# Kernel optimization log

Hardware: AMD Instinct MI355X
Metric: run time of the kernel (lower is better)

The kernel has to match this reference:

```python
import jax, jax.numpy as jnp
import numpy as np


def setup_inputs() -> dict:
    key = jax.random.key(0)
    ks = jax.random.split(key, 6)
    B, S, H, HD = 2, 2048, 2048, 128
    scale = 0.02
    return {
        "hidden_state": jax.random.normal(ks[0], (B, S, H), jnp.float32),
        "attention_mask": jnp.ones((B, 1, 1, S), jnp.int32),
        "Wq": jax.random.normal(ks[1], (H, H), jnp.float32) * scale,
        "bq": jnp.zeros((H,), jnp.float32),
        "Wk": jax.random.normal(ks[2], (HD, H), jnp.float32) * scale,
        "bk": jnp.zeros((HD,), jnp.float32),
        "Wv": jax.random.normal(ks[3], (HD, H), jnp.float32) * scale,
        "bv": jnp.zeros((HD,), jnp.float32),
        "Wo": jax.random.normal(ks[4], (H, H), jnp.float32) * scale,
        "bo": jnp.zeros((H,), jnp.float32),
    }


def reference(hidden_state, attention_mask, Wq, bq, Wk, bk, Wv, bv, Wo, bo):
    B, S, H = hidden_state.shape
    hd = Wk.shape[0]          # head_dim (single shared KV head)
    nh = H // hd              # num query heads
    # projections (torch Linear: x @ W.T + b)
    q = (hidden_state @ Wq.T + bq).reshape(B, S, nh, hd).transpose(0, 2, 1, 3)  # (B,nh,S,hd)
    k = hidden_state @ Wk.T + bk   # (B,S,hd) shared head
    v = hidden_state @ Wv.T + bv   # (B,S,hd)
    scores = jnp.einsum('bhqd,bkd->bhqk', q, k) / jnp.sqrt(jnp.float32(hd))
    scores = jnp.where(attention_mask == 0, -jnp.inf, scores)
    probs = jax.nn.softmax(scores, axis=-1)
    # dropout p=0.0 -> identity (inference)
    out = jnp.einsum('bhqk,bkd->bhqd', probs, v)           # (B,nh,S,hd)
    out = out.transpose(0, 2, 1, 3).reshape(B, S, H)
    return out @ Wo.T + bo
```

## Files before the change

kernel.cpp:

```cpp
#include <hip/hip_runtime.h>

typedef unsigned short u16;
typedef unsigned int u32;
typedef __attribute__((ext_vector_type(8))) short bf16x8;
typedef __attribute__((ext_vector_type(4))) float f32x4;
typedef __attribute__((ext_vector_type(16))) float f32x16;

#define QSC 0.12751798f

__device__ __forceinline__ u16 f2bf(float f) {
  union { float f; unsigned u; } a; a.f = f;
  unsigned r = a.u + 0x7fffu + ((a.u >> 16) & 1u);
  return (u16)(r >> 16);
}

__device__ __forceinline__ void gload16(const void* g, void* l) {
  __builtin_amdgcn_global_load_lds(
      (const __attribute__((address_space(1))) unsigned int*)g,
      (__attribute__((address_space(3))) unsigned int*)l, 16, 0, 0);
}

__global__ __launch_bounds__(256) void cvt_all_k(
    const float* __restrict__ h, const float* __restrict__ wq,
    const float* __restrict__ wk, const float* __restrict__ wv,
    const float* __restrict__ wo, u16* __restrict__ hid,
    u16* __restrict__ wqkv, u16* __restrict__ wob) {
  int i = blockIdx.x * 256 + threadIdx.x;
  if (i >= 4325376) return;
  const float4* s;
  ushort4* d;
  if (i < 2097152) {
    s = (const float4*)h + i;              d = (ushort4*)hid + i;
  } else if (i < 3145728) {
    s = (const float4*)wq + (i - 2097152); d = (ushort4*)wqkv + (i - 2097152);
  } else if (i < 3211264) {
    s = (const float4*)wk + (i - 3145728);
    d = (ushort4*)(wqkv + 4194304) + (i - 3145728);
  } else if (i < 3276800) {
    s = (const float4*)wv + (i - 3211264);
    d = (ushort4*)(wqkv + 4456448) + (i - 3211264);
  } else {
    s = (const float4*)wo + (i - 3276800); d = (ushort4*)wob + (i - 3276800);
  }
  float4 v = *s;
  ushort4 o;
  o.x = f2bf(v.x); o.y = f2bf(v.y); o.z = f2bf(v.z); o.w = f2bf(v.w);
  *d = o;
}

template <int MODE>
__global__ __launch_bounds__(256) void gemm_bt_k(
    const u16* __restrict__ A, const u16* __restrict__ Bm,
    const float* __restrict__ bias0, const float* __restrict__ bias1,
    const float* __restrict__ bias2,
    float* __restrict__ outF, u16* __restrict__ outQ,
    u16* __restrict__ outK, u16* __restrict__ outVt,
    int M, int N, int K) {
  __shared__ u16 As[128 * 32];
  __shared__ u16 Bs[128 * 32];
  const int t = threadIdx.x;
  const int lane = t & 63, wid = t >> 6;
  const int m0 = blockIdx.y * 128, n0 = blockIdx.x * 128;
  const int wr = (wid >> 1) * 64, wc = (wid & 1) * 64;
  const int col = lane & 15, grp = lane >> 4;

  const int srow = t >> 2;
  const int sp = t & 3;
  const int sslot = (sp ^ ((srow >> 1) & 3)) * 8;
  const u16* aS0 = A + (size_t)(m0 + srow) * K + sslot;
  const u16* aS1 = A + (size_t)(m0 + srow + 64) * K + sslot;
  const u16* bS0 = Bm + (size_t)(n0 + srow) * K + sslot;
  const u16* bS1 = Bm + (size_t)(n0 + srow + 64) * K + sslot;
  u16* aD0 = As + t * 8; u16* aD1 = As + (256 + t) * 8;
  u16* bD0 = Bs + t * 8; u16* bD1 = Bs + (256 + t) * 8;

  f32x4 acc[4][4] = {};
  const int nk = K >> 5;
  for (int kt = 0; kt < nk; ++kt) {
    __syncthreads();
    const int ko = kt * 32;
    gload16(aS0 + ko, aD0);
    gload16(aS1 + ko, aD1);
    gload16(bS0 + ko, bD0);
    gload16(bS1 + ko, bD1);
    __syncthreads();
    bf16x8 af[4], bfr[4];
#pragma unroll
    for (int f = 0; f < 4; ++f) {
      int ra = wr + f * 16 + col;
      af[f] = *(const bf16x8*)(const void*)((const char*)As + ra * 64 +
                                            ((grp ^ ((ra >> 1) & 3)) << 4));
      int rb = wc + f * 16 + col;
      bfr[f] = *(const bf16x8*)(const void*)((const char*)Bs + rb * 64 +
                                             ((grp ^ ((rb >> 1) & 3)) << 4));
    }
    __builtin_amdgcn_s_setprio(1);
#pragma unroll
    for (int i = 0; i < 4; ++i)
#pragma unroll
      for (int j = 0; j < 4; ++j)
        acc[i][j] = __builtin_amdgcn_mfma_f32_16x16x32_bf16(af[i], bfr[j],
                                                            acc[i][j], 0, 0, 0);
    __builtin_amdgcn_s_setprio(0);
  }

#pragma unroll
  for (int i = 0; i < 4; ++i) {
    const int gmb = m0 + wr + i * 16 + grp * 4;
#pragma unroll
    for (int j = 0; j < 4; ++j) {
      const int gn = n0 + wc + j * 16 + col;
      float bv;
      if (MODE == 1) bv = bias0[gn];
      else bv = (gn < 2048) ? bias0[gn]
                            : (gn < 2176 ? bias1[gn - 2048] : bias2[gn - 2176]);
#pragma unroll
      for (int r = 0; r < 4; ++r) {
        const int gm = gmb + r;
        float val = acc[i][j][r] + bv;
        if (MODE == 1) {
          outF[(size_t)gm * N + gn] = val;
        } else {
          if (gn < 2048) {
            outQ[(size_t)gm * 2048 + gn] = f2bf(val * QSC);
          } else if (gn < 2176) {
            outK[(size_t)gm * 128 + (gn - 2048)] = f2bf(val);
          } else {
            const int b = gm >> 11, s = gm & 2047, d = gn - 2176;
            outVt[((size_t)(b * 128 + d) << 11) + s] = f2bf(val);
          }
        }
      }
    }
  }
}

__global__ __launch_bounds__(256, 2) void attn_k(const u16* __restrict__ Q,
                                                 const u16* __restrict__ Kb,
                                                 const u16* __restrict__ Vt,
                                                 u16* __restrict__ O) {
  __shared__ u16 Ks[2][64 * 128];
  __shared__ u16 Vs[2][128 * 64];
  const int t = threadIdx.x, lane = t & 63, w = t >> 6;
  const int qt = blockIdx.x & 15;
  const int h = (blockIdx.x >> 4) & 15;
  const int b = blockIdx.x >> 8;
  const int l31 = lane & 31, hi = lane >> 5;
  const int swl = l31 & 7;
  const int q0w = qt * 128 + w * 32;

  bf16x8 qf[8];
  {
    const u16* qp = Q + (size_t)(b * 2048 + q0w + l31) * 2048 + h * 128 + hi * 8;
#pragma unroll
    for (int kc = 0; kc < 8; ++kc) qf[kc] = *(const bf16x8*)(qp + kc * 16);
  }

  const int krow = t >> 4, kslot = t & 15;
  const int sig = (krow & 3) | ((krow & 4) << 1) | ((krow & 8) >> 1);
  const int vrow = t >> 3, vslot = t & 7;
  const u16* ksrc0 =
      Kb + (size_t)(b * 2048 + sig) * 128 + ((kslot ^ (krow & 7)) * 8);
  const u16* vsrc0 =
      Vt + (size_t)(b * 128 + vrow) * 2048 + ((vslot ^ (vrow & 7)) * 8);
  const int ldst = t * 8;

  auto STAGE_K = [&](int ktn, int nb) {
#pragma unroll
    for (int i = 0; i < 4; ++i)
      gload16(ksrc0 + i * 2048 + ktn * 8192, &Ks[nb][i * 2048 + ldst]);
  };
  auto STAGE_V = [&](int ktn, int nb) {
#pragma unroll
    for (int i = 0; i < 4; ++i)
      gload16(vsrc0 + (size_t)i * 65536 + ktn * 64, &Vs[nb][i * 2048 + ldst]);
  };

  STAGE_K(0, 0);
  STAGE_V(0, 0);
  STAGE_K(1, 1);
  __syncthreads();

  f32x16 st0 = {}, st1 = {};
#pragma unroll
  for (int kc = 0; kc < 8; ++kc) {
    const int sw = ((kc * 2 + hi) ^ swl) << 4;
    bf16x8 k0 = *(const bf16x8*)(const void*)((const char*)Ks[0] + l31 * 256 + sw);
    bf16x8 k1 = *(const bf16x8*)(const void*)((const char*)Ks[0] + (32 + l31) * 256 + sw);
    st0 = __builtin_amdgcn_mfma_f32_32x32x16_bf16(k0, qf[kc], st0, 0, 0, 0);
    st1 = __builtin_amdgcn_mfma_f32_32x32x16_bf16(k1, qf[kc], st1, 0, 0, 0);
  }
  STAGE_V(1, 1);
  __syncthreads();

  f32x16 of[4] = {};
  float mrun = -3e38f, lsum = 0.f;
  u32 pk[4][4];

  for (int tt = 0; tt < 31; ++tt) {
    if (tt < 30) STAGE_K(tt + 2, tt & 1);

    const char* kbase = (const char*)Ks[(tt + 1) & 1];
    const char* vbase = (const char*)Vs[tt & 1];
    f32x16 n0 = {}, n1 = {};
#pragma unroll
    for (int kc = 0; kc < 8; ++kc) {
      const int sw = ((kc * 2 + hi) ^ swl) << 4;
      bf16x8 k0 = *(const bf16x8*)(const void*)(kbase + l31 * 256 + sw);
      bf16x8 k1 = *(const bf16x8*)(const void*)(kbase + (32 + l31) * 256 + sw);
      n0 = __builtin_amdgcn_mfma_f32_32x32x16_bf16(k0, qf[kc], n0, 0, 0, 0);
      n1 = __builtin_amdgcn_mfma_f32_32x32x16_bf16(k1, qf[kc], n1, 0, 0, 0);
    }

    float m8[8];
#pragma unroll
    for (int i = 0; i < 8; ++i)
      m8[i] = fmaxf(fmaxf(st0[i], st0[i + 8]), fmaxf(st1[i], st1[i + 8]));
#pragma unroll
    for (int i = 0; i < 4; ++i) m8[i] = fmaxf(m8[i], m8[i + 4]);
    float mx = fmaxf(fmaxf(m8[0], m8[1]), fmaxf(m8[2], m8[3]));
    mx = fmaxf(mx, __shfl_xor(mx, 32));
    if (__any(mx > mrun + 8.f)) {
      float mnew = fmaxf(mrun, mx);
      float al = __builtin_amdgcn_exp2f(mrun - mnew);
      mrun = mnew;
      lsum *= al;
#pragma unroll
      for (int rr = 0; rr < 16; ++rr) {
        const int rho = (rr & 3) + 8 * (rr >> 2) + 4 * hi;
        float av = __shfl(al, (lane & 32) | rho);
#pragma unroll
        for (int dt = 0; dt < 4; ++dt) of[dt][rr] *= av;
      }
    }
    {
      float ps0 = 0.f, ps1 = 0.f;
#pragma unroll
      for (int a = 0; a < 8; ++a) {
        float e0 = __builtin_amdgcn_exp2f(st0[2 * a] - mrun);
        float e1 = __builtin_amdgcn_exp2f(st0[2 * a + 1] - mrun);
        float e2 = __builtin_amdgcn_exp2f(st1[2 * a] - mrun);
        float e3 = __builtin_amdgcn_exp2f(st1[2 * a + 1] - mrun);
        ps0 += (e0 + e1);
        ps1 += (e2 + e3);
        asm("v_cvt_pk_bf16_f32 %0, %1, %2" : "=v"(pk[a >> 2][a & 3]) : "v"(e0), "v"(e1));
        asm("v_cvt_pk_bf16_f32 %0, %1, %2" : "=v"(pk[2 + (a >> 2)][a & 3]) : "v"(e2), "v"(e3));
      }
      lsum += ps0 + ps1;
    }

    __builtin_amdgcn_s_setprio(1);
#pragma unroll
    for (int kvc = 0; kvc < 4; ++kvc) {
      union { u32 u[4]; bf16x8 v; } pu;
#pragma unroll
      for (int ww = 0; ww < 4; ++ww) pu.u[ww] = pk[kvc][ww];
      const int swv = ((kvc * 2 + hi) ^ swl) << 4;
#pragma unroll
      for (int dt = 0; dt < 4; ++dt) {
        bf16x8 vb = *(const bf16x8*)(const void*)(vbase + (dt * 32 + l31) * 128 + swv);
        of[dt] = __builtin_amdgcn_mfma_f32_32x32x16_bf16(pu.v, vb, of[dt], 0, 0, 0);
      }
    }
    __builtin_amdgcn_s_setprio(0);

    __syncthreads();
    if (tt < 30) STAGE_V(tt + 2, tt & 1);
    st0 = n0;
    st1 = n1;
  }

  {
    float m8[8];
#pragma unroll
    for (int i = 0; i < 8; ++i)
      m8[i] = fmaxf(fmaxf(st0[i], st0[i + 8]), fmaxf(st1[i], st1[i + 8]));
#pragma unroll
    for (int i = 0; i < 4; ++i) m8[i] = fmaxf(m8[i], m8[i + 4]);
    float mx = fmaxf(fmaxf(m8[0], m8[1]), fmaxf(m8[2], m8[3]));
    mx = fmaxf(mx, __shfl_xor(mx, 32));
    if (__any(mx > mrun + 8.f)) {
      float mnew = fmaxf(mrun, mx);
      float al = __builtin_amdgcn_exp2f(mrun - mnew);
      mrun = mnew;
      lsum *= al;
#pragma unroll
      for (int rr = 0; rr < 16; ++rr) {
        const int rho = (rr & 3) + 8 * (rr >> 2) + 4 * hi;
        float av = __shfl(al, (lane & 32) | rho);
#pragma unroll
        for (int dt = 0; dt < 4; ++dt) of[dt][rr] *= av;
      }
    }
    float ps = 0.f;
#pragma unroll
    for (int a = 0; a < 8; ++a) {
      float e0 = __builtin_amdgcn_exp2f(st0[2 * a] - mrun);
      float e1 = __builtin_amdgcn_exp2f(st0[2 * a + 1] - mrun);
      float e2 = __builtin_amdgcn_exp2f(st1[2 * a] - mrun);
      float e3 = __builtin_amdgcn_exp2f(st1[2 * a + 1] - mrun);
      ps += (e0 + e1) + (e2 + e3);
      asm("v_cvt_pk_bf16_f32 %0, %1, %2" : "=v"(pk[a >> 2][a & 3]) : "v"(e0), "v"(e1));
      asm("v_cvt_pk_bf16_f32 %0, %1, %2" : "=v"(pk[2 + (a >> 2)][a & 3]) : "v"(e2), "v"(e3));
    }
    lsum += ps;
    const char* vbase = (const char*)Vs[1];
    __builtin_amdgcn_s_setprio(1);
#pragma unroll
    for (int kvc = 0; kvc < 4; ++kvc) {
      union { u32 u[4]; bf16x8 v; } pu;
#pragma unroll
      for (int ww = 0; ww < 4; ++ww) pu.u[ww] = pk[kvc][ww];
      const int swv = ((kvc * 2 + hi) ^ swl) << 4;
#pragma unroll
      for (int dt = 0; dt < 4; ++dt) {
        bf16x8 vb = *(const bf16x8*)(const void*)(vbase + (dt * 32 + l31) * 128 + swv);
        of[dt] = __builtin_amdgcn_mfma_f32_32x32x16_bf16(pu.v, vb, of[dt], 0, 0, 0);
      }
    }
    __builtin_amdgcn_s_setprio(0);
  }

  float lt = lsum + __shfl_xor(lsum, 32);
  float inv = 1.0f / lt;
#pragma unroll
  for (int rr = 0; rr < 16; ++rr) {
    const int rho = (rr & 3) + 8 * (rr >> 2) + 4 * hi;
    float iv = __shfl(inv, (lane & 32) | rho);
    u16* orow = O + (size_t)(b * 2048 + q0w + rho) * 2048 + h * 128 + l31;
#pragma unroll
    for (int dt = 0; dt < 4; ++dt) orow[dt * 32] = f2bf(of[dt][rr] * iv);
  }
}

extern "C" void kernel_launch(void* const* d_in, const int* in_sizes, int n_in,
                              void* d_out, int out_size, void* d_ws,
                              size_t ws_size, hipStream_t stream) {
  const float* hidden = (const float*)d_in[0];
  const float* Wq = (const float*)d_in[2];
  const float* bq = (const float*)d_in[3];
  const float* Wk = (const float*)d_in[4];
  const float* bk = (const float*)d_in[5];
  const float* Wv = (const float*)d_in[6];
  const float* bv = (const float*)d_in[7];
  const float* Wo = (const float*)d_in[8];
  const float* bo = (const float*)d_in[9];
  float* out = (float*)d_out;

  char* ws = (char*)d_ws;
  u16* hid  = (u16*)(ws);
  u16* wqkv = (u16*)(ws + 16777216);
  u16* wo   = (u16*)(ws + 26214400);
  u16* q    = (u16*)(ws + 34603008);
  u16* kb   = (u16*)(ws + 51380224);
  u16* vt   = (u16*)(ws + 52428800);
  u16* attn = (u16*)(ws + 53477376);

  cvt_all_k<<<16896, 256, 0, stream>>>(hidden, Wq, Wk, Wv, Wo, hid, wqkv, wo);

  gemm_bt_k<0><<<dim3(18, 32), 256, 0, stream>>>(
      hid, wqkv, bq, bk, bv, nullptr, q, kb, vt, 4096, 2304, 2048);

  attn_k<<<512, 256, 0, stream>>>(q, kb, vt, attn);

  gemm_bt_k<1><<<dim3(16, 32), 256, 0, stream>>>(
      attn, wo, bo, nullptr, nullptr, out, nullptr, nullptr, nullptr,
      4096, 2048, 2048);
}
```

Before: 210.4 us.

## Load K tiles directly from global into registers instead of LDS staging

K tiles are no longer staged through shared memory. Each lane reads its K fragments straight from global memory into registers, prefetching the next tile right after the QK MFMAs. The software-pipelined QK-ahead structure and the peeled final iteration are removed, so each iteration now computes its own scores. This frees half the LDS and cuts LDS traffic, but it adds register pressure (16 extra bf16x8 fragments) and exposes global-load latency, which may now stall the next iteration's MFMAs.

After: 271.0 us. 1.29x slower.

```diff
diff --git a/kernel.cpp b/kernel.cpp
--- a/kernel.cpp
+++ b/kernel.cpp
@@ -139,7 +139,6 @@
                                                  const u16* __restrict__ Kb,
                                                  const u16* __restrict__ Vt,
                                                  u16* __restrict__ O) {
-  __shared__ u16 Ks[2][64 * 128];
   __shared__ u16 Vs[2][128 * 64];
   const int t = threadIdx.x, lane = t & 63, w = t >> 6;
   const int qt = blockIdx.x & 15;
@@ -156,40 +155,27 @@
     for (int kc = 0; kc < 8; ++kc) qf[kc] = *(const bf16x8*)(qp + kc * 16);
   }
 
-  const int krow = t >> 4, kslot = t & 15;
-  const int sig = (krow & 3) | ((krow & 4) << 1) | ((krow & 8) >> 1);
+  const int sigl = (l31 & 19) | ((l31 & 4) << 1) | ((l31 & 8) >> 1);
+  const u16* kp0 = Kb + (size_t)(b * 2048 + sigl) * 128 + hi * 8;
+  const u16* kp1 = kp0 + 32 * 128;
+
   const int vrow = t >> 3, vslot = t & 7;
-  const u16* ksrc0 =
-      Kb + (size_t)(b * 2048 + sig) * 128 + ((kslot ^ (krow & 7)) * 8);
   const u16* vsrc0 =
       Vt + (size_t)(b * 128 + vrow) * 2048 + ((vslot ^ (vrow & 7)) * 8);
   const int ldst = t * 8;
-
-  auto STAGE_K = [&](int ktn, int nb) {
-#pragma unroll
-    for (int i = 0; i < 4; ++i)
-      gload16(ksrc0 + i * 2048 + ktn * 8192, &Ks[nb][i * 2048 + ldst]);
-  };
   auto STAGE_V = [&](int ktn, int nb) {
 #pragma unroll
     for (int i = 0; i < 4; ++i)
       gload16(vsrc0 + (size_t)i * 65536 + ktn * 64, &Vs[nb][i * 2048 + ldst]);
   };
 
-  STAGE_K(0, 0);
+  bf16x8 kf0[8], kf1[8];
+#pragma unroll
+  for (int kc = 0; kc < 8; ++kc) {
+    kf0[kc] = *(const bf16x8*)(kp0 + kc * 16);
+    kf1[kc] = *(const bf16x8*)(kp1 + kc * 16);
+  }
   STAGE_V(0, 0);
-  STAGE_K(1, 1);
-  __syncthreads();
-
-  f32x16 st0 = {}, st1 = {};
-#pragma unroll
-  for (int kc = 0; kc < 8; ++kc) {
-    const int sw = ((kc * 2 + hi) ^ swl) << 4;
-    bf16x8 k0 = *(const bf16x8*)(const void*)((const char*)Ks[0] + l31 * 256 + sw);
-    bf16x8 k1 = *(const bf16x8*)(const void*)((const char*)Ks[0] + (32 + l31) * 256 + sw);
-    st0 = __builtin_amdgcn_mfma_f32_32x32x16_bf16(k0, qf[kc], st0, 0, 0, 0);
-    st1 = __builtin_amdgcn_mfma_f32_32x32x16_bf16(k1, qf[kc], st1, 0, 0, 0);
-  }
   STAGE_V(1, 1);
   __syncthreads();
 
@@ -197,19 +183,24 @@
   float mrun = -3e38f, lsum = 0.f;
   u32 pk[4][4];
 
-  for (int tt = 0; tt < 31; ++tt) {
-    if (tt < 30) STAGE_K(tt + 2, tt & 1);
-
-    const char* kbase = (const char*)Ks[(tt + 1) & 1];
-    const char* vbase = (const char*)Vs[tt & 1];
-    f32x16 n0 = {}, n1 = {};
+  for (int tt = 0; tt < 32; ++tt) {
+    f32x16 st0 = {}, st1 = {};
+    __builtin_amdgcn_s_setprio(1);
 #pragma unroll
     for (int kc = 0; kc < 8; ++kc) {
-      const int sw = ((kc * 2 + hi) ^ swl) << 4;
-      bf16x8 k0 = *(const bf16x8*)(const void*)(kbase + l31 * 256 + sw);
-      bf16x8 k1 = *(const bf16x8*)(const void*)(kbase + (32 + l31) * 256 + sw);
-      n0 = __builtin_amdgcn_mfma_f32_32x32x16_bf16(k0, qf[kc], n0, 0, 0, 0);
-      n1 = __builtin_amdgcn_mfma_f32_32x32x16_bf16(k1, qf[kc], n1, 0, 0, 0);
+      st0 = __builtin_amdgcn_mfma_f32_32x32x16_bf16(kf0[kc], qf[kc], st0, 0, 0, 0);
+      st1 = __builtin_amdgcn_mfma_f32_32x32x16_bf16(kf1[kc], qf[kc], st1, 0, 0, 0);
+    }
+    __builtin_amdgcn_s_setprio(0);
+
+    if (tt < 31) {
+      const u16* p0 = kp0 + (tt + 1) * 8192;
+      const u16* p1 = kp1 + (tt + 1) * 8192;
+#pragma unroll
+      for (int kc = 0; kc < 8; ++kc) {
+        kf0[kc] = *(const bf16x8*)(p0 + kc * 16);
+        kf1[kc] = *(const bf16x8*)(p1 + kc * 16);
+      }
     }
 
     float m8[8];
@@ -249,6 +240,7 @@
       lsum += ps0 + ps1;
     }
 
+    const char* vbase = (const char*)Vs[tt & 1];
     __builtin_amdgcn_s_setprio(1);
 #pragma unroll
     for (int kvc = 0; kvc < 4; ++kvc) {
@@ -266,59 +258,6 @@
 
     __syncthreads();
     if (tt < 30) STAGE_V(tt + 2, tt & 1);
-    st0 = n0;
-    st1 = n1;
-  }
-
-  {
-    float m8[8];
-#pragma unroll
-    for (int i = 0; i < 8; ++i)
-      m8[i] = fmaxf(fmaxf(st0[i], st0[i + 8]), fmaxf(st1[i], st1[i + 8]));
-#pragma unroll
-    for (int i = 0; i < 4; ++i) m8[i] = fmaxf(m8[i], m8[i + 4]);
-    float mx = fmaxf(fmaxf(m8[0], m8[1]), fmaxf(m8[2], m8[3]));
-    mx = fmaxf(mx, __shfl_xor(mx, 32));
-    if (__any(mx > mrun + 8.f)) {
-      float mnew = fmaxf(mrun, mx);
-      float al = __builtin_amdgcn_exp2f(mrun - mnew);
-      mrun = mnew;
-      lsum *= al;
-#pragma unroll
-      for (int rr = 0; rr < 16; ++rr) {
-        const int rho = (rr & 3) + 8 * (rr >> 2) + 4 * hi;
-        float av = __shfl(al, (lane & 32) | rho);
-#pragma unroll
-        for (int dt = 0; dt < 4; ++dt) of[dt][rr] *= av;
-      }
-    }
-    float ps = 0.f;
-#pragma unroll
-    for (int a = 0; a < 8; ++a) {
-      float e0 = __builtin_amdgcn_exp2f(st0[2 * a] - mrun);
-      float e1 = __builtin_amdgcn_exp2f(st0[2 * a + 1] - mrun);
-      float e2 = __builtin_amdgcn_exp2f(st1[2 * a] - mrun);
-      float e3 = __builtin_amdgcn_exp2f(st1[2 * a + 1] - mrun);
-      ps += (e0 + e1) + (e2 + e3);
-      asm("v_cvt_pk_bf16_f32 %0, %1, %2" : "=v"(pk[a >> 2][a & 3]) : "v"(e0), "v"(e1));
-      asm("v_cvt_pk_bf16_f32 %0, %1, %2" : "=v"(pk[2 + (a >> 2)][a & 3]) : "v"(e2), "v"(e3));
-    }
-    lsum += ps;
-    const char* vbase = (const char*)Vs[1];
-    __builtin_amdgcn_s_setprio(1);
-#pragma unroll
-    for (int kvc = 0; kvc < 4; ++kvc) {
-      union { u32 u[4]; bf16x8 v; } pu;
-#pragma unroll
-      for (int ww = 0; ww < 4; ++ww) pu.u[ww] = pk[kvc][ww];
-      const int swv = ((kvc * 2 + hi) ^ swl) << 4;
-#pragma unroll
-      for (int dt = 0; dt < 4; ++dt) {
-        bf16x8 vb = *(const bf16x8*)(const void*)(vbase + (dt * 32 + l31) * 128 + swv);
-        of[dt] = __builtin_amdgcn_mfma_f32_32x32x16_bf16(pu.v, vb, of[dt], 0, 0, 0);
-      }
-    }
-    __builtin_amdgcn_s_setprio(0);
   }
 
   float lt = lsum + __shfl_xor(lsum, 32);
```
